# Optimization experiments

Hardware: AMD Instinct MI355X
Metric: run time of the kernel (lower is better)

## Reference

```python
import jax, jax.numpy as jnp
import numpy as np

N_NODES = 200000   # graph size
D = 128            # input feature dim
B = 1024           # seed batch
MAX_DEG = 128      # padded adjacency width
HID = 128          # aggregator output_dim (concat -> 2*HID)
N_CLASSES = 64
N_SAMPLES = (25, 10)  # fanout per hop (layer_specs n_train_samples)


def setup_inputs() -> dict:
    key = jax.random.key(0)
    ks = jax.random.split(key, 9)
    ids = jax.random.randint(ks[0], (B,), 0, N_NODES)
    feats = jax.random.normal(ks[1], (N_NODES, D), jnp.float32)
    adj = jax.random.randint(ks[2], (N_NODES, MAX_DEG), 0, N_NODES)
    init = lambda k, shp, fan: jax.random.normal(k, shp, jnp.float32) / np.float32(np.sqrt(fan))
    W_x1 = init(ks[3], (D, HID), D)
    W_n1 = init(ks[4], (D, HID), D)
    W_x2 = init(ks[5], (2 * HID, HID), 2 * HID)
    W_n2 = init(ks[6], (2 * HID, HID), 2 * HID)
    fc_w = init(ks[7], (2 * HID, N_CLASSES), 2 * HID)
    fc_b = jnp.zeros((N_CLASSES,), jnp.float32)
    return dict(ids=ids, feats=feats, adj=adj, W_x1=W_x1, W_n1=W_n1,
                W_x2=W_x2, W_n2=W_n2, fc_w=fc_w, fc_b=fc_b)


def _sample_ids(ids, adj):
    """Multi-hop uniform neighbor sampling (UniformNeighborSampler)."""
    key = jax.random.key(42)
    all_ids = [ids]
    cur = ids
    for i, n in enumerate(N_SAMPLES):
        k = jax.random.fold_in(key, i)
        cols = jax.random.randint(k, (cur.shape[0], n), 0, adj.shape[1])
        cur = adj[cur[:, None], cols].reshape(-1)  # [len(cur)*n]
        all_ids.append(cur)
    return all_ids


def _mean_agg(x, neibs, Wx, Wn, act):
    # neibs: [x.shape[0]*n_samples, d] -> mean over sampled neighbors
    agg = neibs.reshape(x.shape[0], -1, neibs.shape[1]).mean(axis=1)
    out = jnp.concatenate([x @ Wx, agg @ Wn], axis=1)  # bias-free Linears
    return jax.nn.relu(out) if act else out


def reference(ids, feats, adj, W_x1, W_n1, W_x2, W_n2, fc_w, fc_b):
    all_ids = _sample_ids(ids, adj)
    hs = [feats[i] for i in all_ids]  # gather: [B,d], [B*25,d], [B*250,d]
    hs = [_mean_agg(hs[k], hs[k + 1], W_x1, W_n1, True) for k in range(len(hs) - 1)]
    hs = [_mean_agg(hs[k], hs[k + 1], W_x2, W_n2, False) for k in range(len(hs) - 1)]
    out = hs[0]
    # F.normalize(out, dim=1) with eps=1e-12
    out = out / jnp.clip(jnp.linalg.norm(out, axis=1, keepdims=True), 1e-12)
    return out @ fc_w + fc_b
```

## Files before the change

### kernel.cpp

```cpp
#include <hip/hip_runtime.h>
#include <stdint.h>
#include <stddef.h>


typedef short bf16x8v __attribute__((ext_vector_type(8)));
typedef float f32x4v __attribute__((ext_vector_type(4)));

__host__ __device__ inline void tf2x32(uint32_t k0, uint32_t k1,
                                       uint32_t x0, uint32_t x1,
                                       uint32_t &o0, uint32_t &o1)
{
    uint32_t ks2 = k0 ^ k1 ^ 0x1BD11BDAu;
    uint32_t v0 = x0 + k0, v1 = x1 + k1;
#define TFR(d) { v0 += v1; v1 = (v1 << (d)) | (v1 >> (32 - (d))); v1 ^= v0; }
    TFR(13) TFR(15) TFR(26) TFR(6)   v0 += k1;  v1 += ks2 + 1u;
    TFR(17) TFR(29) TFR(16) TFR(24)  v0 += ks2; v1 += k0 + 2u;
    TFR(13) TFR(15) TFR(26) TFR(6)   v0 += k0;  v1 += k1 + 3u;
    TFR(17) TFR(29) TFR(16) TFR(24)  v0 += k1;  v1 += ks2 + 4u;
    TFR(13) TFR(15) TFR(26) TFR(6)   v0 += ks2; v1 += k0 + 5u;
#undef TFR
    o0 = v0; o1 = v1;
}

__device__ inline uint16_t f32_to_bf16_rne(float f)
{
    uint32_t u = __float_as_uint(f);
    u += 0x7FFFu + ((u >> 16) & 1u);
    return (uint16_t)(u >> 16);
}
__device__ inline float bf16_to_f32(uint16_t h)
{
    return __uint_as_float(((uint32_t)h) << 16);
}

__global__ void prologue_kernel(const int* __restrict__ ids, const int* __restrict__ adj,
                                const float* __restrict__ Wx1, const float* __restrict__ Wn1,
                                uint16_t* __restrict__ xh, uint16_t* __restrict__ xl,
                                uint16_t* __restrict__ nh, uint16_t* __restrict__ nl,
                                uint32_t s0a, uint32_t s0b, uint32_t s1a, uint32_t s1b,
                                int* __restrict__ ids1, int* __restrict__ ids2,
                                float4* __restrict__ m2z)
{
    int t = blockIdx.x * 256 + threadIdx.x;
    if (t < 32768) {
        int k = (t & 16383) >> 7, n = t & 127;
        const float* W = (t < 16384) ? Wx1 : Wn1;
        uint16_t* H = (t < 16384) ? xh : nh;
        uint16_t* L = (t < 16384) ? xl : nl;
        float v = W[k * 128 + n];
        uint16_t h = f32_to_bf16_rne(v);
        uint16_t l = f32_to_bf16_rne(v - bf16_to_f32(h));
        H[n * 128 + k] = h;
        L[n * 128 + k] = l;
    } else if (t < 98304) {
        m2z[t - 32768] = make_float4(0.f, 0.f, 0.f, 0.f);
    } else if (t < 123904) {
        int j = t - 98304;
        uint32_t h, l;
        tf2x32(s0a, s0b, 0u, (uint32_t)j, h, l);
        int s1 = adj[(size_t)ids[j / 25] * 128u + ((h ^ l) & 127u)];
        ids1[j] = s1;
        const int* arow = adj + (size_t)s1 * 128u;
        int* o = ids2 + (size_t)j * 10;
#pragma unroll
        for (int u = 0; u < 10; ++u) {
            uint32_t hh, ll;
            tf2x32(s1a, s1b, 0u, (uint32_t)(j * 10 + u), hh, ll);
            o[u] = arow[(hh ^ ll) & 127u];
        }
    }
}

__launch_bounds__(512)
__global__ void gemm_fused(const float* __restrict__ feats, const int* __restrict__ ids,
                           const int* __restrict__ ids1, const int* __restrict__ ids2,
                           const uint16_t* __restrict__ xh, const uint16_t* __restrict__ xl,
                           const uint16_t* __restrict__ nh, const uint16_t* __restrict__ nl,
                           float* __restrict__ m2, float* __restrict__ h10)
{
    __shared__ __align__(16) char smem[34816];
    uint16_t (*Ahi)[136] = reinterpret_cast<uint16_t(*)[136]>(smem);
    uint16_t (*Alo)[136] = reinterpret_cast<uint16_t(*)[136]>(smem + 17408);

    const int tid = threadIdx.x;
    const int vb = blockIdx.x;
    int z, bx;
    if (vb < 400)      { z = 1; bx = vb; }
    else if (vb < 416) { z = 3; bx = vb - 400; }
    else if (vb < 816) { z = 0; bx = vb - 416; }
    else               { z = 2; bx = vb - 816; }
    const int rb = bx * 64;
    const bool isX = (z == 0) || (z == 2);
    const uint16_t* WH = isX ? xh : nh;
    const uint16_t* WL = isX ? xl : nl;
    const int ccol0 = isX ? 0 : 128;

    const int lane = tid & 63;
    const int wv = tid >> 6;

    if (isX) {
        const int* g = (z == 0) ? ids1 : ids;
#pragma unroll
        for (int i = 0; i < 4; ++i) {
            int s = tid + i * 512;
            int row = s >> 5, f4 = s & 31, k0 = f4 * 4;
            size_t arow = (size_t)g[rb + row];
            float4 v = *(const float4*)(feats + arow * 128 + k0);
            uint16_t h0 = f32_to_bf16_rne(v.x), h1 = f32_to_bf16_rne(v.y);
            uint16_t h2 = f32_to_bf16_rne(v.z), h3 = f32_to_bf16_rne(v.w);
            *(ushort4*)&Ahi[row][k0] = make_ushort4(h0, h1, h2, h3);
            *(ushort4*)&Alo[row][k0] = make_ushort4(f32_to_bf16_rne(v.x - bf16_to_f32(h0)),
                                                    f32_to_bf16_rne(v.y - bf16_to_f32(h1)),
                                                    f32_to_bf16_rne(v.z - bf16_to_f32(h2)),
                                                    f32_to_bf16_rne(v.w - bf16_to_f32(h3)));
        }
    } else {
        const int h = lane & 31;
        const int hw = tid >> 5;
        const int FAN = (z == 1) ? 10 : 25;
        const int* src = (z == 1) ? ids2 : ids1;
        const float sc = (z == 1) ? 0.1f : (1.0f / 25.0f);
        int idv[4];
#pragma unroll
        for (int j = 0; j < 4; ++j) {
            int r = rb + hw * 4 + j;
            idv[j] = (h < FAN) ? src[(size_t)r * FAN + h] : 0;
        }
#pragma unroll
        for (int j = 0; j < 4; ++j) {
            float a0 = 0.f, a1 = 0.f, a2 = 0.f, a3 = 0.f;
            if (z == 1) {
#pragma unroll
                for (int t = 0; t < 10; ++t) {
                    int id = __shfl(idv[j], (lane & 32) + t, 64);
                    float4 vv = *((const float4*)(feats + (size_t)id * 128) + h);
                    a0 += vv.x; a1 += vv.y; a2 += vv.z; a3 += vv.w;
                }
            } else {
#pragma unroll
                for (int t = 0; t < 25; ++t) {
                    int id = __shfl(idv[j], (lane & 32) + t, 64);
                    float4 vv = *((const float4*)(feats + (size_t)id * 128) + h);
                    a0 += vv.x; a1 += vv.y; a2 += vv.z; a3 += vv.w;
                }
            }
            a0 *= sc; a1 *= sc; a2 *= sc; a3 *= sc;
            uint16_t b0 = f32_to_bf16_rne(a0), b1 = f32_to_bf16_rne(a1);
            uint16_t b2 = f32_to_bf16_rne(a2), b3 = f32_to_bf16_rne(a3);
            int row = hw * 4 + j;
            *(ushort4*)&Ahi[row][h * 4] = make_ushort4(b0, b1, b2, b3);
            *(ushort4*)&Alo[row][h * 4] =
                make_ushort4(f32_to_bf16_rne(a0 - bf16_to_f32(b0)),
                             f32_to_bf16_rne(a1 - bf16_to_f32(b1)),
                             f32_to_bf16_rne(a2 - bf16_to_f32(b2)),
                             f32_to_bf16_rne(a3 - bf16_to_f32(b3)));
        }
    }
    __syncthreads();

    const int wm = (wv >> 2) * 32;
    const int wn = (wv & 3) * 32;
    const int fr = lane & 15;
    const int kb = lane >> 4;

    f32x4v acc[2][2] = {};
#pragma unroll
    for (int ks = 0; ks < 4; ++ks) {
        const int kk = ks * 32 + kb * 8;
        bf16x8v aH[2], aL[2];
#pragma unroll
        for (int mi = 0; mi < 2; ++mi) {
            aH[mi] = *(const bf16x8v*)&Ahi[wm + mi * 16 + fr][kk];
            aL[mi] = *(const bf16x8v*)&Alo[wm + mi * 16 + fr][kk];
        }
#pragma unroll
        for (int ni = 0; ni < 2; ++ni) {
            size_t wrow = (size_t)(wn + ni * 16 + fr) * 128 + kk;
            bf16x8v bH = *(const bf16x8v*)(WH + wrow);
            bf16x8v bL = *(const bf16x8v*)(WL + wrow);
#pragma unroll
            for (int mi = 0; mi < 2; ++mi) {
                acc[mi][ni] = __builtin_amdgcn_mfma_f32_16x16x32_bf16(aH[mi], bH, acc[mi][ni], 0, 0, 0);
                acc[mi][ni] = __builtin_amdgcn_mfma_f32_16x16x32_bf16(aH[mi], bL, acc[mi][ni], 0, 0, 0);
                acc[mi][ni] = __builtin_amdgcn_mfma_f32_16x16x32_bf16(aL[mi], bH, acc[mi][ni], 0, 0, 0);
            }
        }
    }

    if (z < 2) {
        __syncthreads();
        float (*Red)[132] = reinterpret_cast<float(*)[132]>(smem);
#pragma unroll
        for (int mi = 0; mi < 2; ++mi)
#pragma unroll
            for (int ni = 0; ni < 2; ++ni) {
                int rl = wm + mi * 16 + kb * 4;
                int cl = wn + ni * 16 + fr;
#pragma unroll
                for (int r = 0; r < 4; ++r)
                    Red[rl + r][cl] = fmaxf(acc[mi][ni][r], 0.0f);
            }
        __syncthreads();
        int col = tid & 127;
        for (int gg = rb / 25 + (tid >> 7); gg * 25 < rb + 64; gg += 4) {
            int rs = max(gg * 25, rb), re = min(gg * 25 + 25, rb + 64);
            float s = 0.f;
            for (int r = rs; r < re; ++r) s += Red[r - rb][col];
            atomicAdd(&m2[(size_t)gg * 256 + ccol0 + col], s * (1.0f / 25.0f));
        }
    } else {
#pragma unroll
        for (int mi = 0; mi < 2; ++mi)
#pragma unroll
            for (int ni = 0; ni < 2; ++ni) {
                int orow = rb + wm + mi * 16 + kb * 4;
                int ocol = ccol0 + wn + ni * 16 + fr;
#pragma unroll
                for (int r = 0; r < 4; ++r)
                    h10[(size_t)(orow + r) * 256 + ocol] = fmaxf(acc[mi][ni][r], 0.0f);
            }
    }
}

__launch_bounds__(256)
__global__ void tail_kernel(const float* __restrict__ h10, const float* __restrict__ m2,
                            const float* __restrict__ Wx2, const float* __restrict__ Wn2,
                            const float* __restrict__ fcw, const float* __restrict__ fcb,
                            float* __restrict__ out)
{
    __shared__ float X[4][260];
    __shared__ float M[4][260];
    __shared__ float H[4][260];
    const int tid = threadIdx.x;
    const int r0 = blockIdx.x * 4;

    {
        int r = tid >> 6, q = tid & 63;
        *(float4*)&X[r][q * 4] = *((const float4*)(h10 + (size_t)(r0 + r) * 256) + q);
        *(float4*)&M[r][q * 4] = *((const float4*)(m2 + (size_t)(r0 + r) * 256) + q);
    }
    __syncthreads();

    {
        const float* W = (tid < 128) ? Wx2 : Wn2;
        const float (*S)[260] = (tid < 128) ? X : M;
        int c = tid & 127;
        float acc0 = 0.f, acc1 = 0.f, acc2 = 0.f, acc3 = 0.f;
        for (int k4 = 0; k4 < 256; k4 += 4) {
            float4 s0 = *(const float4*)&S[0][k4];
            float4 s1 = *(const float4*)&S[1][k4];
            float4 s2 = *(const float4*)&S[2][k4];
            float4 s3 = *(const float4*)&S[3][k4];
            float w0 = W[(size_t)(k4 + 0) * 128 + c];
            float w1 = W[(size_t)(k4 + 1) * 128 + c];
            float w2 = W[(size_t)(k4 + 2) * 128 + c];
            float w3 = W[(size_t)(k4 + 3) * 128 + c];
            acc0 = fmaf(s0.x, w0, fmaf(s0.y, w1, fmaf(s0.z, w2, fmaf(s0.w, w3, acc0))));
            acc1 = fmaf(s1.x, w0, fmaf(s1.y, w1, fmaf(s1.z, w2, fmaf(s1.w, w3, acc1))));
            acc2 = fmaf(s2.x, w0, fmaf(s2.y, w1, fmaf(s2.z, w2, fmaf(s2.w, w3, acc2))));
            acc3 = fmaf(s3.x, w0, fmaf(s3.y, w1, fmaf(s3.z, w2, fmaf(s3.w, w3, acc3))));
        }
        H[0][tid] = acc0; H[1][tid] = acc1; H[2][tid] = acc2; H[3][tid] = acc3;
    }
    __syncthreads();

    const int w = tid >> 6, lane = tid & 63;
    float4 hv = *((const float4*)&H[w][0] + lane);
    float ss = hv.x * hv.x + hv.y * hv.y + hv.z * hv.z + hv.w * hv.w;
#pragma unroll
    for (int o = 32; o > 0; o >>= 1) ss += __shfl_xor(ss, o, 64);
    float scale = 1.0f / fmaxf(sqrtf(ss), 1e-12f);

    float acc = 0.f;
    for (int k4 = 0; k4 < 256; k4 += 4) {
        float4 h4 = *(const float4*)&H[w][k4];
        acc = fmaf(h4.x, fcw[(size_t)(k4 + 0) * 64 + lane],
              fmaf(h4.y, fcw[(size_t)(k4 + 1) * 64 + lane],
              fmaf(h4.z, fcw[(size_t)(k4 + 2) * 64 + lane],
              fmaf(h4.w, fcw[(size_t)(k4 + 3) * 64 + lane], acc))));
    }
    out[(size_t)(r0 + w) * 64 + lane] = acc * scale + fcb[lane];
}

extern "C" void kernel_launch(void* const* d_in, const int* in_sizes, int n_in,
                              void* d_out, int out_size, void* d_ws, size_t ws_size,
                              hipStream_t stream)
{
    const int*   ids   = (const int*)d_in[0];
    const float* feats = (const float*)d_in[1];
    const int*   adj   = (const int*)d_in[2];
    const float* W_x1  = (const float*)d_in[3];
    const float* W_n1  = (const float*)d_in[4];
    const float* W_x2  = (const float*)d_in[5];
    const float* W_n2  = (const float*)d_in[6];
    const float* fc_w  = (const float*)d_in[7];
    const float* fc_b  = (const float*)d_in[8];
    float* out = (float*)d_out;

    char* ws = (char*)d_ws;
    int*      ids1 = (int*)(ws + 0);
    int*      ids2 = (int*)(ws + 102400);
    float*    h10  = (float*)(ws + 1126400);
    float*    m2   = (float*)(ws + 2174976);
    uint16_t* xh   = (uint16_t*)(ws + 3223552);
    uint16_t* xl   = (uint16_t*)(ws + 3256320);
    uint16_t* nh   = (uint16_t*)(ws + 3289088);
    uint16_t* nl   = (uint16_t*)(ws + 3321856);

    uint32_t f0a, f0b, f1a, f1b, s0a, s0b, s1a, s1b;
    tf2x32(0u, 42u, 0u, 0u, f0a, f0b);
    tf2x32(0u, 42u, 0u, 1u, f1a, f1b);
    tf2x32(f0a, f0b, 0u, 1u, s0a, s0b);
    tf2x32(f1a, f1b, 0u, 1u, s1a, s1b);

    prologue_kernel<<<484, 256, 0, stream>>>(ids, adj, W_x1, W_n1,
                                             xh, xl, nh, nl,
                                             s0a, s0b, s1a, s1b,
                                             ids1, ids2, (float4*)m2);
    gemm_fused<<<832, 512, 0, stream>>>(feats, ids, ids1, ids2,
                                        xh, xl, nh, nl, m2, h10);
    tail_kernel<<<256, 256, 0, stream>>>(h10, m2, W_x2, W_n2, fc_w, fc_b, out);
}
```

Before: 62.64 us.

## Fuse tail kernel into GEMM kernel via global completion counter

Removes the separate tail kernel launch by having the last 256 blocks of the fused GEMM kernel spin on a global atomic counter until all 832 blocks finish, then run the second-layer aggregation, normalization and classifier in reused shared memory. The prologue zeroes the counter. This saves a launch gap, but the spin-wait relies on every block being co-resident or already scheduled, which is a deadlock risk if waiting blocks occupy CUs while earlier blocks are still pending.

```diff
diff --git a/kernel.cpp b/kernel.cpp
--- a/kernel.cpp
+++ b/kernel.cpp
@@ -39,7 +39,7 @@
                                 uint16_t* __restrict__ nh, uint16_t* __restrict__ nl,
                                 uint32_t s0a, uint32_t s0b, uint32_t s1a, uint32_t s1b,
                                 int* __restrict__ ids1, int* __restrict__ ids2,
-                                float4* __restrict__ m2z)
+                                float4* __restrict__ m2z, int* __restrict__ done)
 {
     int t = blockIdx.x * 256 + threadIdx.x;
     if (t < 32768) {
@@ -68,6 +68,8 @@
             tf2x32(s1a, s1b, 0u, (uint32_t)(j * 10 + u), hh, ll);
             o[u] = arow[(hh ^ ll) & 127u];
         }
+    } else if (t == 123904) {
+        *done = 0;
     }
 }
 
@@ -76,7 +78,10 @@
                            const int* __restrict__ ids1, const int* __restrict__ ids2,
                            const uint16_t* __restrict__ xh, const uint16_t* __restrict__ xl,
                            const uint16_t* __restrict__ nh, const uint16_t* __restrict__ nl,
-                           float* __restrict__ m2, float* __restrict__ h10)
+                           float* __restrict__ m2, float* __restrict__ h10,
+                           const float* __restrict__ Wx2, const float* __restrict__ Wn2,
+                           const float* __restrict__ fcw, const float* __restrict__ fcb,
+                           float* __restrict__ out, int* __restrict__ done)
 {
     __shared__ __align__(16) char smem[34816];
     uint16_t (*Ahi)[136] = reinterpret_cast<uint16_t(*)[136]>(smem);
@@ -220,28 +225,32 @@
                     h10[(size_t)(orow + r) * 256 + ocol] = fmaxf(acc[mi][ni][r], 0.0f);
             }
     }
-}
-
-__launch_bounds__(256)
-__global__ void tail_kernel(const float* __restrict__ h10, const float* __restrict__ m2,
-                            const float* __restrict__ Wx2, const float* __restrict__ Wn2,
-                            const float* __restrict__ fcw, const float* __restrict__ fcb,
-                            float* __restrict__ out)
-{
-    __shared__ float X[4][260];
-    __shared__ float M[4][260];
-    __shared__ float H[4][260];
-    const int tid = threadIdx.x;
-    const int r0 = blockIdx.x * 4;
-
-    {
+
+    __syncthreads();
+    __threadfence();
+    if (tid == 0) atomicAdd(done, 1);
+
+    if (vb < 576) return;
+
+    if (tid == 0) {
+        while (atomicAdd(done, 0) < 832) { }
+    }
+    __syncthreads();
+    __threadfence();
+
+    float (*X)[260] = reinterpret_cast<float(*)[260]>(smem);
+    float (*M)[260] = reinterpret_cast<float(*)[260]>(smem + 4160);
+    float (*H)[260] = reinterpret_cast<float(*)[260]>(smem + 8320);
+    const int r0 = (vb - 576) * 4;
+
+    if (tid < 256) {
         int r = tid >> 6, q = tid & 63;
         *(float4*)&X[r][q * 4] = *((const float4*)(h10 + (size_t)(r0 + r) * 256) + q);
         *(float4*)&M[r][q * 4] = *((const float4*)(m2 + (size_t)(r0 + r) * 256) + q);
     }
     __syncthreads();
 
-    {
+    if (tid < 256) {
         const float* W = (tid < 128) ? Wx2 : Wn2;
         const float (*S)[260] = (tid < 128) ? X : M;
         int c = tid & 127;
@@ -264,22 +273,24 @@
     }
     __syncthreads();
 
-    const int w = tid >> 6, lane = tid & 63;
-    float4 hv = *((const float4*)&H[w][0] + lane);
-    float ss = hv.x * hv.x + hv.y * hv.y + hv.z * hv.z + hv.w * hv.w;
-#pragma unroll
-    for (int o = 32; o > 0; o >>= 1) ss += __shfl_xor(ss, o, 64);
-    float scale = 1.0f / fmaxf(sqrtf(ss), 1e-12f);
-
-    float acc = 0.f;
-    for (int k4 = 0; k4 < 256; k4 += 4) {
-        float4 h4 = *(const float4*)&H[w][k4];
-        acc = fmaf(h4.x, fcw[(size_t)(k4 + 0) * 64 + lane],
-              fmaf(h4.y, fcw[(size_t)(k4 + 1) * 64 + lane],
-              fmaf(h4.z, fcw[(size_t)(k4 + 2) * 64 + lane],
-              fmaf(h4.w, fcw[(size_t)(k4 + 3) * 64 + lane], acc))));
-    }
-    out[(size_t)(r0 + w) * 64 + lane] = acc * scale + fcb[lane];
+    if (tid < 256) {
+        const int w = tid >> 6, ln = tid & 63;
+        float4 hv = *((const float4*)&H[w][0] + ln);
+        float ss = hv.x * hv.x + hv.y * hv.y + hv.z * hv.z + hv.w * hv.w;
+#pragma unroll
+        for (int o = 32; o > 0; o >>= 1) ss += __shfl_xor(ss, o, 64);
+        float scale = 1.0f / fmaxf(sqrtf(ss), 1e-12f);
+
+        float acc = 0.f;
+        for (int k4 = 0; k4 < 256; k4 += 4) {
+            float4 h4 = *(const float4*)&H[w][k4];
+            acc = fmaf(h4.x, fcw[(size_t)(k4 + 0) * 64 + ln],
+                  fmaf(h4.y, fcw[(size_t)(k4 + 1) * 64 + ln],
+                  fmaf(h4.z, fcw[(size_t)(k4 + 2) * 64 + ln],
+                  fmaf(h4.w, fcw[(size_t)(k4 + 3) * 64 + ln], acc))));
+        }
+        out[(size_t)(r0 + w) * 64 + ln] = acc * scale + fcb[ln];
+    }
 }
 
 extern "C" void kernel_launch(void* const* d_in, const int* in_sizes, int n_in,
@@ -306,6 +317,7 @@
     uint16_t* xl   = (uint16_t*)(ws + 3256320);
     uint16_t* nh   = (uint16_t*)(ws + 3289088);
     uint16_t* nl   = (uint16_t*)(ws + 3321856);
+    int*      done = (int*)(ws + 3354624);
 
     uint32_t f0a, f0b, f1a, f1b, s0a, s0b, s1a, s1b;
     tf2x32(0u, 42u, 0u, 0u, f0a, f0b);
@@ -313,11 +325,11 @@
     tf2x32(f0a, f0b, 0u, 1u, s0a, s0b);
     tf2x32(f1a, f1b, 0u, 1u, s1a, s1b);
 
-    prologue_kernel<<<484, 256, 0, stream>>>(ids, adj, W_x1, W_n1,
+    prologue_kernel<<<485, 256, 0, stream>>>(ids, adj, W_x1, W_n1,
                                              xh, xl, nh, nl,
                                              s0a, s0b, s1a, s1b,
-                                             ids1, ids2, (float4*)m2);
+                                             ids1, ids2, (float4*)m2, done);
     gemm_fused<<<832, 512, 0, stream>>>(feats, ids, ids1, ids2,
-                                        xh, xl, nh, nl, m2, h10);
-    tail_kernel<<<256, 256, 0, stream>>>(h10, m2, W_x2, W_n2, fc_w, fc_b, out);
-}
+                                        xh, xl, nh, nl, m2, h10,
+                                        W_x2, W_n2, fc_w, fc_b, out, done);
+}
```

Result: slower. 244.3 us (+290.0%).
